# Kernel tuning notes

Measured on AMD Instinct MI355X. Metric: run time of the kernel, lower is better.

The kernel has to match this reference:

```python
import jax, jax.numpy as jnp
import numpy as np

B, S, E, H = 2, 2048, 1024, 16
D = E // H  # head_dim = 64
MASKED_BIAS = -10000.0


def setup_inputs() -> dict:
    key = jax.random.key(0)
    k1, k2, k3 = jax.random.split(key, 3)
    return {
        "hidden_states": jax.random.normal(k1, (B, S, E), dtype=jnp.float32),
        "w_attn": jax.random.normal(k2, (E, 3 * E), dtype=jnp.float32) * 0.02,
        "b_attn": jnp.zeros((3 * E,), dtype=jnp.float32),
        "w_proj": jax.random.normal(k3, (E, E), dtype=jnp.float32) * 0.02,
        "b_proj": jnp.zeros((E,), dtype=jnp.float32),
    }


def reference(hidden_states, w_attn, b_attn, w_proj, b_proj):
    # c_attn: [B,S,E] @ [E,3E] + bias
    qkv = hidden_states @ w_attn + b_attn
    q, k, v = jnp.split(qkv, 3, axis=-1)

    def split_heads(t):  # [B,S,E] -> [B,H,S,D]
        return t.reshape(B, S, H, D).transpose(0, 2, 1, 3)

    q, k, v = split_heads(q), split_heads(k), split_heads(v)

    # scores: [B,H,S,S], scaled by sqrt(head_dim)
    scores = jnp.einsum("bhqd,bhkd->bhqk", q, k) / jnp.float32(D) ** 0.5
    causal = jnp.tril(jnp.ones((S, S), dtype=bool))
    scores = jnp.where(causal, scores, jnp.float32(MASKED_BIAS))
    attn_weights = jax.nn.softmax(scores, axis=-1)
    # dropout p=0 (eval): identity
    attn_out = jnp.einsum("bhqk,bhkd->bhqd", attn_weights, v)
    # merge heads: [B,H,S,D] -> [B,S,E]
    attn_out = attn_out.transpose(0, 2, 1, 3).reshape(B, S, E)
    attn_out = attn_out @ w_proj + b_proj
    return attn_out, attn_weights
```

## Files before the change

kernel.cpp:

```cpp
#include <hip/hip_runtime.h>


typedef unsigned short u16;
typedef __attribute__((ext_vector_type(8))) short bf16x8;
typedef __attribute__((ext_vector_type(4))) float f32x4;
typedef __attribute__((ext_vector_type(4))) unsigned short u16x4;

#define MFMA(a, b, c) __builtin_amdgcn_mfma_f32_16x16x32_bf16((a), (b), (c), 0, 0, 0)

typedef const __attribute__((address_space(1))) void* gas_t;
typedef __attribute__((address_space(3))) void* las_t;
__device__ __forceinline__ void async_copy16(const void* g, void* l) {
  __builtin_amdgcn_global_load_lds((gas_t)g, (las_t)l, 16, 0, 0);
}

__device__ __forceinline__ u16 f2bf(float f) {
  unsigned u = __builtin_bit_cast(unsigned, f);
  u += 0x7FFFu + ((u >> 16) & 1u);
  return (u16)(u >> 16);
}
__device__ __forceinline__ float E2(float x) { return __builtin_amdgcn_exp2f(x); }

#define QSCALE 0.18033688011112042f

__global__ __launch_bounds__(256) void k_cast(const float* __restrict__ in,
                                              u16* __restrict__ out, int n) {
  int i = (blockIdx.x * 256 + threadIdx.x) * 4;
  if (i + 3 < n) {
    float4 v = *(const float4*)(in + i);
    u16x4 o = { f2bf(v.x), f2bf(v.y), f2bf(v.z), f2bf(v.w) };
    *(u16x4*)(out + i) = o;
  }
}

__global__ __launch_bounds__(256) void k_transpose_cast(const float* __restrict__ in,
                                                        u16* __restrict__ out,
                                                        int Kd, int Nd) {
  __shared__ float tile[64][65];
  int n0 = blockIdx.x * 64, k0 = blockIdx.y * 64;
  int t = threadIdx.x, col = t & 63, r4 = t >> 6;
#pragma unroll
  for (int ph = 0; ph < 16; ++ph) {
    int row = ph * 4 + r4;
    tile[row][col] = in[(size_t)(k0 + row) * Nd + n0 + col];
  }
  __syncthreads();
#pragma unroll
  for (int ph = 0; ph < 16; ++ph) {
    int row = ph * 4 + r4;
    out[(size_t)(n0 + row) * Kd + k0 + col] = f2bf(tile[col][row]);
  }
}

__global__ __launch_bounds__(256) void k_transpose_v(const u16* __restrict__ V,
                                                     u16* __restrict__ Vt) {
  __shared__ u16 tile[64][65];
  int bh = blockIdx.y, s0 = blockIdx.x * 64;
  int t = threadIdx.x, col = t & 63, r4 = t >> 6;
#pragma unroll
  for (int ph = 0; ph < 16; ++ph) {
    int row = ph * 4 + r4;
    tile[row][col] = V[((size_t)bh * 2048 + s0 + row) * 64 + col];
  }
  __syncthreads();
#pragma unroll
  for (int ph = 0; ph < 16; ++ph) {
    int row = ph * 4 + r4;
    Vt[((size_t)bh * 64 + row) * 2048 + s0 + col] = tile[col][row];
  }
}

#define GEMM_PROLOG()                                                          \
  __shared__ u16 As[128 * 32];                                                 \
  __shared__ u16 Bs[128 * 32];                                                 \
  int t = threadIdx.x;                                                         \
  int wave = t >> 6, lane = t & 63, quad = lane >> 4, l16 = lane & 15;         \
  int wm = wave >> 1, wn = wave & 1;                                           \
  int m0 = blockIdx.y * 128, n0 = blockIdx.x * 128;                            \
      \
  int f1 = wave * 64 + lane, f2 = f1 + 256;                                    \
  const u16* gA1 = A + (size_t)(m0 + (f1 >> 2)) * 1024 + (f1 & 3) * 8;         \
  const u16* gA2 = A + (size_t)(m0 + (f2 >> 2)) * 1024 + (f2 & 3) * 8;         \
  const u16* gB1 = Bt + (size_t)(n0 + (f1 >> 2)) * 1024 + (f1 & 3) * 8;        \
  const u16* gB2 = Bt + (size_t)(n0 + (f2 >> 2)) * 1024 + (f2 & 3) * 8;        \
  u16* lA1 = As + wave * 512;               \
  u16* lA2 = As + 2048 + wave * 512;                                           \
  u16* lB1 = Bs + wave * 512;                                                  \
  u16* lB2 = Bs + 2048 + wave * 512;                                           \
  f32x4 acc[4][4];                                                             \
  for (int i = 0; i < 4; ++i)                                                  \
    for (int j = 0; j < 4; ++j) acc[i][j] = (f32x4){0.f, 0.f, 0.f, 0.f};       \
  for (int k0 = 0; k0 < 1024; k0 += 32) {                                      \
    async_copy16(gA1 + k0, lA1);                                               \
    async_copy16(gA2 + k0, lA2);                                               \
    async_copy16(gB1 + k0, lB1);                                               \
    async_copy16(gB2 + k0, lB2);                                               \
    __syncthreads();                                                           \
    bf16x8 fa[4], fb[4];                                                       \
    _Pragma("unroll") for (int i = 0; i < 4; ++i)                              \
        fa[i] = *(const bf16x8*)(As + (wm * 64 + i * 16 + l16) * 32 + quad * 8);\
    _Pragma("unroll") for (int j = 0; j < 4; ++j)                              \
        fb[j] = *(const bf16x8*)(Bs + (wn * 64 + j * 16 + l16) * 32 + quad * 8);\
    _Pragma("unroll") for (int i = 0; i < 4; ++i)                              \
      _Pragma("unroll") for (int j = 0; j < 4; ++j)                            \
          acc[i][j] = MFMA(fa[i], fb[j], acc[i][j]);                           \
    __syncthreads();                                                           \
  }

__global__ __launch_bounds__(256) void k_gemm_qkv(const u16* __restrict__ A,
                                                  const u16* __restrict__ Bt,
                                                  const float* __restrict__ bias,
                                                  u16* __restrict__ Q,
                                                  u16* __restrict__ Kp,
                                                  u16* __restrict__ V) {
  GEMM_PROLOG()
#pragma unroll
  for (int j = 0; j < 4; ++j) {
    int n = n0 + wn * 64 + j * 16 + l16;
    float bv = bias[n];
    int which = n >> 10, e = n & 1023, h = e >> 6, d = e & 63;
#pragma unroll
    for (int i = 0; i < 4; ++i)
#pragma unroll
      for (int r = 0; r < 4; ++r) {
        int m = m0 + wm * 64 + i * 16 + quad * 4 + r;
        int b = m >> 11, s = m & 2047;
        float v = acc[i][j][r] + bv;
        size_t off = ((size_t)((b * 16 + h) * 2048 + s)) * 64 + d;
        if (which == 0)      Q[off]  = f2bf(v * QSCALE);
        else if (which == 1) Kp[off] = f2bf(v);
        else                 V[off]  = f2bf(v);
      }
  }
}

__global__ __launch_bounds__(256) void k_gemm_proj(const u16* __restrict__ A,
                                                   const u16* __restrict__ Bt,
                                                   const float* __restrict__ bias,
                                                   float* __restrict__ out) {
  GEMM_PROLOG()
#pragma unroll
  for (int j = 0; j < 4; ++j) {
    int n = n0 + wn * 64 + j * 16 + l16;
    float bv = bias[n];
#pragma unroll
    for (int i = 0; i < 4; ++i)
#pragma unroll
      for (int r = 0; r < 4; ++r) {
        int m = m0 + wm * 64 + i * 16 + quad * 4 + r;
        out[(size_t)m * 1024 + n] = acc[i][j][r] + bv;
      }
  }
}

__global__ __launch_bounds__(256) void k_attn(const u16* __restrict__ Q,
                                              const u16* __restrict__ Kp,
                                              const u16* __restrict__ Vt,
                                              u16* __restrict__ ctx,
                                              float* __restrict__ Wout) {
  __shared__ float Pf[4][16 * 36];
  __shared__ u16 Pb[4][16][40];
  int t = threadIdx.x;
  int w = t >> 6, lane = t & 63, quad = lane >> 4, l16 = lane & 15;
  int bh = blockIdx.y;
  int q0 = (gridDim.x - 1 - blockIdx.x) * 64 + w * 16;

  const u16* qrow = Q + ((size_t)bh * 2048 + q0 + l16) * 64 + quad * 8;
  bf16x8 aq0 = *(const bf16x8*)(qrow);
  bf16x8 aq1 = *(const bf16x8*)(qrow + 32);

  const u16* kbase = Kp + (size_t)bh * 2048 * 64;
  float m[4] = {-1e30f, -1e30f, -1e30f, -1e30f};
  float l[4] = {0.f, 0.f, 0.f, 0.f};
  int qmax = q0 + 15;
  int nt1 = q0 / 16 + 1;

  for (int kt = 0; kt < nt1; ++kt) {
    const u16* kr = kbase + (size_t)(kt * 16 + l16) * 64 + quad * 8;
    bf16x8 b0 = *(const bf16x8*)(kr);
    bf16x8 b1 = *(const bf16x8*)(kr + 32);
    f32x4 c = {0.f, 0.f, 0.f, 0.f};
    c = MFMA(aq0, b0, c);
    c = MFMA(aq1, b1, c);
    int col = kt * 16 + l16;
#pragma unroll
    for (int r = 0; r < 4; ++r) {
      int q = q0 + quad * 4 + r;
      float v = (col <= q) ? c[r] : -1e30f;
      float nm = fmaxf(m[r], v);
      l[r] = l[r] * E2(m[r] - nm) + E2(v - nm);
      m[r] = nm;
    }
  }
#pragma unroll
  for (int r = 0; r < 4; ++r) {
#pragma unroll
    for (int off = 1; off < 16; off <<= 1) {
      float om = __shfl_xor(m[r], off, 16);
      float ol = __shfl_xor(l[r], off, 16);
      float nm = fmaxf(m[r], om);
      l[r] = l[r] * E2(m[r] - nm) + ol * E2(om - nm);
      m[r] = nm;
    }
  }
  float rl[4];
#pragma unroll
  for (int r = 0; r < 4; ++r) rl[r] = 1.f / l[r];

  f32x4 oacc[4];
#pragma unroll
  for (int s4 = 0; s4 < 4; ++s4) oacc[s4] = (f32x4){0.f, 0.f, 0.f, 0.f};
  u16* pw = &Pb[w][0][0];
  float* pf = &Pf[w][0];
  const u16* vtb = Vt + (size_t)bh * 64 * 2048;
  float* wrow = Wout + (size_t)bh * 2048 * 2048;
  int srow = lane >> 3, scol = (lane & 7) << 2;

  int na = qmax / 32 + 1;
  for (int kt2 = 0; kt2 < na; ++kt2) {
    int k0 = kt2 * 32;
    f32x4 cc[2] = {{0.f,0.f,0.f,0.f}, {0.f,0.f,0.f,0.f}};
    const u16* kr = kbase + (size_t)(k0 + l16) * 64 + quad * 8;
    bf16x8 b00 = *(const bf16x8*)(kr);
    bf16x8 b01 = *(const bf16x8*)(kr + 32);
    const u16* kr2 = kr + 16 * 64;
    bf16x8 b10 = *(const bf16x8*)(kr2);
    bf16x8 b11 = *(const bf16x8*)(kr2 + 32);
    cc[0] = MFMA(aq0, b00, cc[0]);
    cc[0] = MFMA(aq1, b01, cc[0]);
    cc[1] = MFMA(aq0, b10, cc[1]);
    cc[1] = MFMA(aq1, b11, cc[1]);
#pragma unroll
    for (int sub = 0; sub < 2; ++sub) {
      int col = k0 + sub * 16 + l16;
#pragma unroll
      for (int r = 0; r < 4; ++r) {
        int q = q0 + quad * 4 + r;
        float p = (col <= q) ? E2(cc[sub][r] - m[r]) * rl[r] : 0.f;
        pf[(quad * 4 + r) * 36 + sub * 16 + l16] = p;
        pw[(quad * 4 + r) * 40 + sub * 16 + l16] = f2bf(p);
      }
    }
    f32x4 v0 = *(const f32x4*)(pf + srow * 36 + scol);
    f32x4 v1 = *(const f32x4*)(pf + (srow + 8) * 36 + scol);
    *(f32x4*)(wrow + (size_t)(q0 + srow) * 2048 + k0 + scol) = v0;
    *(f32x4*)(wrow + (size_t)(q0 + srow + 8) * 2048 + k0 + scol) = v1;
    bf16x8 pa = *(const bf16x8*)(pw + l16 * 40 + quad * 8);
#pragma unroll
    for (int s4 = 0; s4 < 4; ++s4) {
      const u16* vr = vtb + (size_t)(s4 * 16 + l16) * 2048 + k0 + quad * 8;
      bf16x8 bv = *(const bf16x8*)(vr);
      oacc[s4] = MFMA(pa, bv, oacc[s4]);
    }
  }
  int zstart = na * 32;
  f32x4 z = {0.f, 0.f, 0.f, 0.f};
  for (int r = 0; r < 16; ++r) {
    float* rb = wrow + (size_t)(q0 + r) * 2048;
    for (int c = zstart + (lane << 2); c < 2048; c += 256)
      *(f32x4*)(rb + c) = z;
  }
  int b = bh >> 4, h = bh & 15;
#pragma unroll
  for (int s4 = 0; s4 < 4; ++s4)
#pragma unroll
    for (int r = 0; r < 4; ++r) {
      int q = q0 + quad * 4 + r;
      int d = s4 * 16 + l16;
      ctx[((size_t)(b * 2048 + q)) * 1024 + h * 64 + d] = f2bf(oacc[s4][r]);
    }
}

extern "C" void kernel_launch(void* const* d_in, const int* in_sizes, int n_in,
                              void* d_out, int out_size, void* d_ws, size_t ws_size,
                              hipStream_t stream) {
  const float* hs     = (const float*)d_in[0];
  const float* w_attn = (const float*)d_in[1];
  const float* b_attn = (const float*)d_in[2];
  const float* w_proj = (const float*)d_in[3];
  const float* b_proj = (const float*)d_in[4];

  char*  outc  = (char*)d_out;
  float* out_f = (float*)d_out;
  float* Wout  = out_f + 4194304;

  u16* qbuf = (u16*)outc;
  u16* kbuf = (u16*)(outc + 8388608);
  u16* hsb  = (u16*)(outc + 530579456);
  u16* wtA  = (u16*)(outc + 538968064);
  u16* vbuf = (u16*)(outc + 545259520);

  char* ws  = (char*)d_ws;
  u16*  vt  = (u16*)ws;
  u16*  ctx = (u16*)(ws + 8388608);
  u16*  wtP = (u16*)(ws + 16777216);

  k_cast<<<4096, 256, 0, stream>>>(hs, hsb, 4194304);
  k_transpose_cast<<<dim3(48, 16), 256, 0, stream>>>(w_attn, wtA, 1024, 3072);
  k_transpose_cast<<<dim3(16, 16), 256, 0, stream>>>(w_proj, wtP, 1024, 1024);
  k_gemm_qkv<<<dim3(24, 32), 256, 0, stream>>>(hsb, wtA, b_attn, qbuf, kbuf, vbuf);
  k_transpose_v<<<dim3(32, 32), 256, 0, stream>>>(vbuf, vt);
  k_attn<<<dim3(32, 32), 256, 0, stream>>>(qbuf, kbuf, vt, ctx, Wout);
  k_gemm_proj<<<dim3(8, 32), 256, 0, stream>>>(ctx, wtP, b_proj, out_f);
}
```

Baseline: 902.6 us.

## Pipeline K loads, dual softmax stats, balanced query-tile order in attention

The first-pass row-max/sum loop now handles 32 keys per iteration with two independent online-softmax accumulators and prefetches the next K tile into registers, which shortens dependency chains and hides load latency. The block index is remapped to a 1D grid that interleaves heads with a zigzag query-tile order, to balance causal work across CUs. The separate bf16 P buffer in LDS is removed; P is instead read back from the fp32 LDS buffer and converted in registers. Launch bounds request 4 blocks per SM, which may force register spills.

```diff
diff --git a/kernel.cpp b/kernel.cpp
--- a/kernel.cpp
+++ b/kernel.cpp
@@ -77,13 +77,12 @@
   int wave = t >> 6, lane = t & 63, quad = lane >> 4, l16 = lane & 15;         \
   int wm = wave >> 1, wn = wave & 1;                                           \
   int m0 = blockIdx.y * 128, n0 = blockIdx.x * 128;                            \
-      \
   int f1 = wave * 64 + lane, f2 = f1 + 256;                                    \
   const u16* gA1 = A + (size_t)(m0 + (f1 >> 2)) * 1024 + (f1 & 3) * 8;         \
   const u16* gA2 = A + (size_t)(m0 + (f2 >> 2)) * 1024 + (f2 & 3) * 8;         \
   const u16* gB1 = Bt + (size_t)(n0 + (f1 >> 2)) * 1024 + (f1 & 3) * 8;        \
   const u16* gB2 = Bt + (size_t)(n0 + (f2 >> 2)) * 1024 + (f2 & 3) * 8;        \
-  u16* lA1 = As + wave * 512;               \
+  u16* lA1 = As + wave * 512;                                                  \
   u16* lA2 = As + 2048 + wave * 512;                                           \
   u16* lB1 = Bs + wave * 512;                                                  \
   u16* lB2 = Bs + 2048 + wave * 512;                                           \
@@ -153,44 +152,71 @@
   }
 }
 
-__global__ __launch_bounds__(256) void k_attn(const u16* __restrict__ Q,
-                                              const u16* __restrict__ Kp,
-                                              const u16* __restrict__ Vt,
-                                              u16* __restrict__ ctx,
-                                              float* __restrict__ Wout) {
+__global__ __launch_bounds__(256, 4) void k_attn(const u16* __restrict__ Q,
+                                                 const u16* __restrict__ Kp,
+                                                 const u16* __restrict__ Vt,
+                                                 u16* __restrict__ ctx,
+                                                 float* __restrict__ Wout) {
   __shared__ float Pf[4][16 * 36];
-  __shared__ u16 Pb[4][16][40];
   int t = threadIdx.x;
   int w = t >> 6, lane = t & 63, quad = lane >> 4, l16 = lane & 15;
-  int bh = blockIdx.y;
-  int q0 = (gridDim.x - 1 - blockIdx.x) * 64 + w * 16;
+  int id = blockIdx.x;
+  int bh = id & 31;
+  int ii = id >> 5, jj = ii & 7, ss = ii >> 3;
+  int qt = (ss == 0) ? jj : (ss == 1) ? 15 - jj : (ss == 2) ? 16 + jj : 31 - jj;
+  int q0 = qt * 64 + w * 16;
 
   const u16* qrow = Q + ((size_t)bh * 2048 + q0 + l16) * 64 + quad * 8;
   bf16x8 aq0 = *(const bf16x8*)(qrow);
   bf16x8 aq1 = *(const bf16x8*)(qrow + 32);
 
   const u16* kbase = Kp + (size_t)bh * 2048 * 64;
-  float m[4] = {-1e30f, -1e30f, -1e30f, -1e30f};
-  float l[4] = {0.f, 0.f, 0.f, 0.f};
   int qmax = q0 + 15;
-  int nt1 = q0 / 16 + 1;
-
-  for (int kt = 0; kt < nt1; ++kt) {
-    const u16* kr = kbase + (size_t)(kt * 16 + l16) * 64 + quad * 8;
-    bf16x8 b0 = *(const bf16x8*)(kr);
-    bf16x8 b1 = *(const bf16x8*)(kr + 32);
-    f32x4 c = {0.f, 0.f, 0.f, 0.f};
-    c = MFMA(aq0, b0, c);
-    c = MFMA(aq1, b1, c);
-    int col = kt * 16 + l16;
+
+  float m0[4], l0[4], m1[4], l1[4];
+#pragma unroll
+  for (int r = 0; r < 4; ++r) { m0[r] = m1[r] = -1e30f; l0[r] = l1[r] = 0.f; }
+  int nt = (q0 + 47) >> 5;
+
+  const u16* kr0 = kbase + (size_t)l16 * 64 + quad * 8;
+  bf16x8 nb00 = *(const bf16x8*)(kr0);
+  bf16x8 nb01 = *(const bf16x8*)(kr0 + 32);
+  bf16x8 nb10 = *(const bf16x8*)(kr0 + 1024);
+  bf16x8 nb11 = *(const bf16x8*)(kr0 + 1024 + 32);
+  for (int kt = 0; kt < nt; ++kt) {
+    bf16x8 b00 = nb00, b01 = nb01, b10 = nb10, b11 = nb11;
+    if (kt + 1 < nt) {
+      const u16* kn = kbase + (size_t)((kt + 1) * 32 + l16) * 64 + quad * 8;
+      nb00 = *(const bf16x8*)(kn);
+      nb01 = *(const bf16x8*)(kn + 32);
+      nb10 = *(const bf16x8*)(kn + 1024);
+      nb11 = *(const bf16x8*)(kn + 1024 + 32);
+    }
+    f32x4 c0 = {0.f, 0.f, 0.f, 0.f}, c1 = c0;
+    c0 = MFMA(aq0, b00, c0);
+    c0 = MFMA(aq1, b01, c0);
+    c1 = MFMA(aq0, b10, c1);
+    c1 = MFMA(aq1, b11, c1);
+    int col0 = kt * 32 + l16, col1 = col0 + 16;
 #pragma unroll
     for (int r = 0; r < 4; ++r) {
       int q = q0 + quad * 4 + r;
-      float v = (col <= q) ? c[r] : -1e30f;
-      float nm = fmaxf(m[r], v);
-      l[r] = l[r] * E2(m[r] - nm) + E2(v - nm);
-      m[r] = nm;
-    }
+      float v0 = (col0 <= q) ? c0[r] : -1e30f;
+      float nm0 = fmaxf(m0[r], v0);
+      l0[r] = l0[r] * E2(m0[r] - nm0) + E2(v0 - nm0);
+      m0[r] = nm0;
+      float v1 = (col1 <= q) ? c1[r] : -1e30f;
+      float nm1 = fmaxf(m1[r], v1);
+      l1[r] = l1[r] * E2(m1[r] - nm1) + E2(v1 - nm1);
+      m1[r] = nm1;
+    }
+  }
+  float m[4], l[4];
+#pragma unroll
+  for (int r = 0; r < 4; ++r) {
+    float nm = fmaxf(m0[r], m1[r]);
+    l[r] = l0[r] * E2(m0[r] - nm) + l1[r] * E2(m1[r] - nm);
+    m[r] = nm;
   }
 #pragma unroll
   for (int r = 0; r < 4; ++r) {
@@ -210,7 +236,6 @@
   f32x4 oacc[4];
 #pragma unroll
   for (int s4 = 0; s4 < 4; ++s4) oacc[s4] = (f32x4){0.f, 0.f, 0.f, 0.f};
-  u16* pw = &Pb[w][0][0];
   float* pf = &Pf[w][0];
   const u16* vtb = Vt + (size_t)bh * 64 * 2048;
   float* wrow = Wout + (size_t)bh * 2048 * 2048;
@@ -223,9 +248,8 @@
     const u16* kr = kbase + (size_t)(k0 + l16) * 64 + quad * 8;
     bf16x8 b00 = *(const bf16x8*)(kr);
     bf16x8 b01 = *(const bf16x8*)(kr + 32);
-    const u16* kr2 = kr + 16 * 64;
-    bf16x8 b10 = *(const bf16x8*)(kr2);
-    bf16x8 b11 = *(const bf16x8*)(kr2 + 32);
+    bf16x8 b10 = *(const bf16x8*)(kr + 1024);
+    bf16x8 b11 = *(const bf16x8*)(kr + 1024 + 32);
     cc[0] = MFMA(aq0, b00, cc[0]);
     cc[0] = MFMA(aq1, b01, cc[0]);
     cc[1] = MFMA(aq0, b10, cc[1]);
@@ -238,14 +262,20 @@
         int q = q0 + quad * 4 + r;
         float p = (col <= q) ? E2(cc[sub][r] - m[r]) * rl[r] : 0.f;
         pf[(quad * 4 + r) * 36 + sub * 16 + l16] = p;
-        pw[(quad * 4 + r) * 40 + sub * 16 + l16] = f2bf(p);
       }
     }
     f32x4 v0 = *(const f32x4*)(pf + srow * 36 + scol);
     f32x4 v1 = *(const f32x4*)(pf + (srow + 8) * 36 + scol);
     *(f32x4*)(wrow + (size_t)(q0 + srow) * 2048 + k0 + scol) = v0;
     *(f32x4*)(wrow + (size_t)(q0 + srow + 8) * 2048 + k0 + scol) = v1;
-    bf16x8 pa = *(const bf16x8*)(pw + l16 * 40 + quad * 8);
+    f32x4 pa0 = *(const f32x4*)(pf + l16 * 36 + quad * 8);
+    f32x4 pa1 = *(const f32x4*)(pf + l16 * 36 + quad * 8 + 4);
+    bf16x8 pa;
+#pragma unroll
+    for (int e = 0; e < 4; ++e) {
+      pa[e]     = (short)f2bf(pa0[e]);
+      pa[e + 4] = (short)f2bf(pa1[e]);
+    }
 #pragma unroll
     for (int s4 = 0; s4 < 4; ++s4) {
       const u16* vr = vtb + (size_t)(s4 * 16 + l16) * 2048 + k0 + quad * 8;
@@ -300,6 +330,6 @@
   k_transpose_cast<<<dim3(16, 16), 256, 0, stream>>>(w_proj, wtP, 1024, 1024);
   k_gemm_qkv<<<dim3(24, 32), 256, 0, stream>>>(hsb, wtA, b_attn, qbuf, kbuf, vbuf);
   k_transpose_v<<<dim3(32, 32), 256, 0, stream>>>(vbuf, vt);
-  k_attn<<<dim3(32, 32), 256, 0, stream>>>(qbuf, kbuf, vt, ctx, Wout);
+  k_attn<<<1024, 256, 0, stream>>>(qbuf, kbuf, vt, ctx, Wout);
   k_gemm_proj<<<dim3(8, 32), 256, 0, stream>>>(ctx, wtP, b_proj, out_f);
 }
```

Measured after the change: 790.5 us. 1.14x faster.
